# Optimization experiments

Hardware: AMD Instinct MI355X
Metric: run time of the kernel (lower is better)

Reference implementation:

```python
import jax, jax.numpy as jnp
import numpy as np

DEPTH = 6; HEADS = 6; DIM = 384; HD = DIM // HEADS
WS = 14; WINDOW_BLOCKS = (0, 1, 3, 4)
IMG = 512; PATCH = 16; GRID = IMG // PATCH        # 32x32 token grid
PRE_GRID = 14                                      # 224 // 16 pretrain grid
SCALE = HD ** -0.5


def layer_norm(x, w, b, eps=1e-5):
    u = x.mean(-1, keepdims=True)
    s = ((x - u) ** 2).mean(-1, keepdims=True)
    return (x - u) / jnp.sqrt(s + eps) * w + b


def get_rel_pos(size, rel_pos):
    # q_size == k_size here; relative coords in [0, 2*size-2]
    coords = jnp.arange(size)[:, None] - jnp.arange(size)[None, :] + (size - 1)
    return rel_pos[coords]  # (size, size, HD)


def attention(x, qkv_w, qkv_b, proj_w, proj_b, rel_h, rel_w):
    B, H, W, C = x.shape
    N = H * W
    qkv = (x.reshape(B, N, C) @ qkv_w.T + qkv_b).reshape(B, N, 3, HEADS, HD)
    qkv = jnp.moveaxis(qkv, 2, 0).transpose(0, 1, 3, 2, 4)  # (3,B,h,N,d)
    q, k, v = qkv[0], qkv[1], qkv[2]
    attn = jnp.einsum('bhqd,bhkd->bhqk', q * SCALE, k)
    # decomposed relative position bias (ViTDet add_decomposed_rel_pos)
    Rh = get_rel_pos(H, rel_h)  # (H,H,d)
    Rw = get_rel_pos(W, rel_w)  # (W,W,d)
    rq = q.reshape(B, HEADS, H, W, HD)
    bias_h = jnp.einsum('bnhwc,hkc->bnhwk', rq, Rh)  # (B,h,H,W,H)
    bias_w = jnp.einsum('bnhwc,wkc->bnhwk', rq, Rw)  # (B,h,H,W,W)
    attn = (attn.reshape(B, HEADS, H, W, H, W)
            + bias_h[..., :, None] + bias_w[..., None, :]).reshape(B, HEADS, N, N)
    attn = jax.nn.softmax(attn, axis=-1)
    out = jnp.einsum('bhqk,bhkd->bhqd', attn, v)
    out = out.transpose(0, 2, 1, 3).reshape(B, H, W, C)
    return out @ proj_w.T + proj_b


def window_partition(x, ws):
    B, H, W, C = x.shape
    pad_h = (ws - H % ws) % ws
    pad_w = (ws - W % ws) % ws
    x = jnp.pad(x, ((0, 0), (0, pad_h), (0, pad_w), (0, 0)))
    Hp, Wp = H + pad_h, W + pad_w
    x = x.reshape(B, Hp // ws, ws, Wp // ws, ws, C)
    x = x.transpose(0, 1, 3, 2, 4, 5).reshape(-1, ws, ws, C)
    return x, Hp, Wp


def window_unpartition(win, ws, Hp, Wp, H, W):
    B = win.shape[0] // ((Hp // ws) * (Wp // ws))
    x = win.reshape(B, Hp // ws, Wp // ws, ws, ws, -1)
    x = x.transpose(0, 1, 3, 2, 4, 5).reshape(B, Hp, Wp, -1)
    return x[:, :H, :W]


def block(x, p, windowed):
    shortcut = x
    x = layer_norm(x, p['n1w'], p['n1b'])
    if windowed:
        H, W = x.shape[1], x.shape[2]
        x, Hp, Wp = window_partition(x, WS)
    x = attention(x, p['qw'], p['qb'], p['pw'], p['pb'], p['rh'], p['rw'])
    if windowed:
        x = window_unpartition(x, WS, Hp, Wp, H, W)
    x = shortcut + x
    h = layer_norm(x, p['n2w'], p['n2b'])
    h = jax.nn.gelu(h @ p['f1w'].T + p['f1b'], approximate=False)
    return x + h @ p['f2w'].T + p['f2b']


def vit_forward(x, patch_w, patch_b, pos_embed, norm1_w, norm1_b, qkv_w, qkv_b,
                proj_w, proj_b, norm2_w, norm2_b, fc1_w, fc1_b, fc2_w, fc2_b,
                rel_pos_h, rel_pos_w):
    y = jax.lax.conv_general_dilated(
        x, patch_w, (PATCH, PATCH), 'VALID',
        dimension_numbers=('NCHW', 'OIHW', 'NCHW'))
    y = y.transpose(0, 2, 3, 1) + patch_b  # (B, GRID, GRID, DIM)
    # abs pos embed: bicubic resize from pretrain 14x14 grid to 32x32
    pos = pos_embed.reshape(1, PRE_GRID, PRE_GRID, DIM)
    pos = jax.image.resize(pos, (1, GRID, GRID, DIM), 'bicubic')
    y = y + pos
    for i in range(DEPTH):
        windowed = i in WINDOW_BLOCKS
        L = 2 * WS - 1 if windowed else 2 * GRID - 1
        p = dict(n1w=norm1_w[i], n1b=norm1_b[i], qw=qkv_w[i], qb=qkv_b[i],
                 pw=proj_w[i], pb=proj_b[i], rh=rel_pos_h[i, :L], rw=rel_pos_w[i, :L],
                 n2w=norm2_w[i], n2b=norm2_b[i], f1w=fc1_w[i], f1b=fc1_b[i],
                 f2w=fc2_w[i], f2b=fc2_b[i])
        y = block(y, p, windowed)
    return y.transpose(0, 3, 1, 2)  # (B, DIM, GRID, GRID) 'last_feat'


def setup_inputs() -> dict:
    key = jax.random.key(0)
    ks = jax.random.split(key, 10)
    B = 4
    std = 0.02
    f32 = jnp.float32
    return {
        'x': jax.random.normal(ks[0], (B, 3, IMG, IMG), f32),
        'patch_w': jax.random.normal(ks[1], (DIM, 3, PATCH, PATCH), f32) * 0.05,
        'patch_b': jnp.zeros((DIM,), f32),
        'pos_embed': jax.random.normal(ks[2], (1, PRE_GRID * PRE_GRID, DIM), f32) * std,
        'norm1_w': jnp.ones((DEPTH, DIM), f32),
        'norm1_b': jnp.zeros((DEPTH, DIM), f32),
        'qkv_w': jax.random.normal(ks[3], (DEPTH, 3 * DIM, DIM), f32) * std,
        'qkv_b': jnp.zeros((DEPTH, 3 * DIM), f32),
        'proj_w': jax.random.normal(ks[4], (DEPTH, DIM, DIM), f32) * std,
        'proj_b': jnp.zeros((DEPTH, DIM), f32),
        'norm2_w': jnp.ones((DEPTH, DIM), f32),
        'norm2_b': jnp.zeros((DEPTH, DIM), f32),
        'fc1_w': jax.random.normal(ks[5], (DEPTH, 4 * DIM, DIM), f32) * std,
        'fc1_b': jnp.zeros((DEPTH, 4 * DIM), f32),
        'fc2_w': jax.random.normal(ks[6], (DEPTH, DIM, 4 * DIM), f32) * std,
        'fc2_b': jnp.zeros((DEPTH, DIM), f32),
        'rel_pos_h': jax.random.normal(ks[7], (DEPTH, 2 * GRID - 1, HD), f32) * std,
        'rel_pos_w': jax.random.normal(ks[8], (DEPTH, 2 * GRID - 1, HD), f32) * std,
    }


def reference(x, patch_w, patch_b, pos_embed, norm1_w, norm1_b, qkv_w, qkv_b,
              proj_w, proj_b, norm2_w, norm2_b, fc1_w, fc1_b, fc2_w, fc2_b,
              rel_pos_h, rel_pos_w):
    return vit_forward(x, patch_w, patch_b, pos_embed, norm1_w, norm1_b, qkv_w, qkv_b,
                       proj_w, proj_b, norm2_w, norm2_b, fc1_w, fc1_b, fc2_w, fc2_b,
                       rel_pos_h, rel_pos_w)
```

## Files before the change

kernel.cpp:

```cpp
#include <hip/hip_runtime.h>
#include <math.h>

#define B_SZ 4
#define DIM 384
#define HEADS 6
#define HD 64
#define NTOK 4096
#define WS 14
#define NWIN 36
#define WTOK 196

typedef unsigned short u16;
typedef __bf16 bf16_t;
typedef bf16_t bf16x8 __attribute__((ext_vector_type(8)));
typedef float f32x4 __attribute__((ext_vector_type(4)));

__device__ __forceinline__ float bf2f(unsigned u) { return __uint_as_float(u << 16); }
__device__ __forceinline__ u16 f2bf(float f) {
    unsigned u = __float_as_uint(f);
    unsigned r = (u + 0x7fffu + ((u >> 16) & 1u)) >> 16;
    return (u16)r;
}

__device__ __forceinline__ void ldsload16(const u16* g, u16* l) {
    __builtin_amdgcn_global_load_lds(
        (const __attribute__((address_space(1))) unsigned int*)g,
        (__attribute__((address_space(3))) unsigned int*)l, 16, 0, 0);
}

__device__ __forceinline__ int swz(int r) { return (r ^ (r >> 2)) & 3; }

__device__ inline float cubic_keys(float x) {
    x = fabsf(x);
    if (x <= 1.f) return ((1.5f * x - 2.5f) * x) * x + 1.f;
    if (x < 2.f)  return ((-0.5f * x + 2.5f) * x - 4.f) * x + 2.f;
    return 0.f;
}

__global__ __launch_bounds__(256) void setup_kernel(
        const float* __restrict__ p0, const float* __restrict__ p1,
        const float* __restrict__ p2, const float* __restrict__ p3,
        const float* __restrict__ p4, const float* __restrict__ p5,
        u16* __restrict__ wb, const float* __restrict__ pe,
        float* __restrict__ posr, const float* __restrict__ x,
        u16* __restrict__ col) {
    int i = (blockIdx.x * 256 + threadIdx.x) * 4;
    if (i < 10918656) {
        const float* s; int off;
        if      (i <   294912) { s = p0; off = 0; }
        else if (i <  2949120) { s = p1; off = 294912; }
        else if (i <  3833856) { s = p2; off = 2949120; }
        else if (i <  7372800) { s = p3; off = 3833856; }
        else if (i < 10911744) { s = p4; off = 7372800; }
        else                   { s = p5; off = 10911744; }
        float4 v = *(const float4*)(s + (i - off));
        u16 o[4] = { f2bf(v.x), f2bf(v.y), f2bf(v.z), f2bf(v.w) };
        *(uint2*)(wb + i) = *(const uint2*)o;
        return;
    }
    i -= 10918656;
    if (i < 393216) {
        int c = i % 384;
        int g = i / 384;
        int gy = g / 32, gx = g % 32;
        float wy[14], wx[14];
        float sy = (gy + 0.5f) * (14.f / 32.f) - 0.5f;
        float sx = (gx + 0.5f) * (14.f / 32.f) - 0.5f;
        float toty = 0.f, totx = 0.f;
        #pragma unroll
        for (int k = 0; k < 14; ++k) {
            wy[k] = cubic_keys(sy - (float)k); toty += wy[k];
            wx[k] = cubic_keys(sx - (float)k); totx += wx[k];
        }
        float4 acc = {0.f, 0.f, 0.f, 0.f};
        #pragma unroll 1
        for (int iy = 0; iy < 14; ++iy) {
            if (wy[iy] == 0.f) continue;
            float4 row = {0.f, 0.f, 0.f, 0.f};
            for (int ix = 0; ix < 14; ++ix) {
                if (wx[ix] == 0.f) continue;
                float4 pv = *(const float4*)(pe + (iy * 14 + ix) * 384 + c);
                row.x += wx[ix] * pv.x; row.y += wx[ix] * pv.y;
                row.z += wx[ix] * pv.z; row.w += wx[ix] * pv.w;
            }
            acc.x += wy[iy] * row.x; acc.y += wy[iy] * row.y;
            acc.z += wy[iy] * row.z; acc.w += wy[iy] * row.w;
        }
        float inv = 1.f / (toty * totx);
        acc.x *= inv; acc.y *= inv; acc.z *= inv; acc.w *= inv;
        *(float4*)(posr + i) = acc;
        return;
    }
    i -= 393216;
    if (i < 3145728) {
        int kk = i % 768;
        int p  = i / 768;
        int b  = p / 1024;
        int ph = (p % 1024) / 32;
        int pw = p % 32;
        int c = kk / 256;
        int r = kk % 256;
        int ii = r / 16, j = r % 16;
        float4 v = *(const float4*)(x + (size_t)b * 3 * 512 * 512 +
                                    (size_t)c * 512 * 512 +
                                    (size_t)(ph * 16 + ii) * 512 + (pw * 16 + j));
        u16 o[4] = { f2bf(v.x), f2bf(v.y), f2bf(v.z), f2bf(v.w) };
        *(uint2*)(col + i) = *(const uint2*)o;
    }
}

__global__ __launch_bounds__(64) void epi_ln_kernel(const float* __restrict__ P,
        const float* __restrict__ bias, const float* __restrict__ posr,
        float* __restrict__ y, int addy, int nsk,
        const float* __restrict__ lw, const float* __restrict__ lb,
        u16* __restrict__ lnout, float* __restrict__ outT)
{
    int tok = blockIdx.x, t = threadIdx.x;
    size_t base = (size_t)tok * 384;
    float v[6];
    float s = 0.f;
    #pragma unroll
    for (int i = 0; i < 6; ++i) {
        int c = t + 64 * i;
        float val = bias[c];
        #pragma unroll 1
        for (int sk = 0; sk < nsk; ++sk)
            val += P[(size_t)sk * 1572864 + base + c];
        if (posr) val += posr[(size_t)(tok & 1023) * 384 + c];
        if (addy) val += y[base + c];
        v[i] = val; s += val;
    }
    if (outT) {
        int b = tok >> 10, g = tok & 1023;
        #pragma unroll
        for (int i = 0; i < 6; ++i) {
            int c = t + 64 * i;
            outT[((size_t)(b * 384 + c)) * 1024 + g] = v[i];
        }
        return;
    }
    #pragma unroll
    for (int i = 0; i < 6; ++i) y[base + t + 64 * i] = v[i];
    if (!lnout) return;
    #pragma unroll
    for (int off = 32; off > 0; off >>= 1) s += __shfl_xor(s, off);
    float mean = s * (1.f / 384.f);
    float vs = 0.f;
    #pragma unroll
    for (int i = 0; i < 6; ++i) { float d = v[i] - mean; vs += d * d; }
    #pragma unroll
    for (int off = 32; off > 0; off >>= 1) vs += __shfl_xor(vs, off);
    float inv = rsqrtf(vs * (1.f / 384.f) + 1e-5f);
    u16* orow = lnout + base;
    #pragma unroll
    for (int i = 0; i < 6; ++i) {
        int c = t + 64 * i;
        orow[c] = f2bf((v[i] - mean) * inv * lw[c] + lb[c]);
    }
}

__global__ __launch_bounds__(256) void mfma_gemm4(
        const u16* __restrict__ A, const u16* __restrict__ Wt,
        const float* __restrict__ bias,
        float* __restrict__ outf, u16* __restrict__ outb,
        float* __restrict__ outp,
        int M, int N, int K, int act, int ksplit)
{
    __shared__ u16 As[2][8192];
    __shared__ u16 Bs[2][4096];
    int t = threadIdx.x;
    int lane = t & 63, wave = t >> 6;
    int wm = (wave >> 1) * 64, wn = (wave & 1) * 32;
    int m0 = blockIdx.y * 128, n0 = blockIdx.x * 64;
    int ks = blockIdx.z * ksplit;

    int r0 = t >> 2,        c0 = ((t & 3) ^ swz(t >> 2)) * 8;
    int r1 = 64 + (t >> 2), c1 = ((t & 3) ^ swz(64 + (t >> 2))) * 8;
    const u16* a0 = A + (size_t)(m0 + r0) * K + c0;
    const u16* a1 = A + (size_t)(m0 + r1) * K + c1;
    const u16* b0 = Wt + (size_t)(n0 + r0) * K + c0;

    auto stage = [&](int k0, int buf) {
        ldsload16(a0 + k0,      &As[buf][wave * 512]);
        ldsload16(a1 + k0,      &As[buf][2048 + wave * 512]);
        ldsload16(b0 + k0,      &Bs[buf][wave * 512]);
        ldsload16(a0 + k0 + 32, &As[buf][4096 + wave * 512]);
        ldsload16(a1 + k0 + 32, &As[buf][6144 + wave * 512]);
        ldsload16(b0 + k0 + 32, &Bs[buf][2048 + wave * 512]);
    };

    f32x4 acc[4][2] = {};
    int row_a = wm + (lane & 15);
    int row_b = wn + (lane & 15);
    int lq = lane >> 4;
    int nchunks = ksplit / 64;

    stage(ks, 0);
    __syncthreads();

    for (int ci = 0; ci < nchunks; ++ci) {
        int p = ci & 1;
        bool pref = (ci + 1 < nchunks);
        if (pref) stage(ks + (ci + 1) * 64, 1 - p);
        #pragma unroll
        for (int hf = 0; hf < 2; ++hf) {
            bf16x8 af[4], bfr[2];
            #pragma unroll
            for (int i = 0; i < 4; ++i) {
                int r = row_a + i * 16;
                af[i] = *(const bf16x8*)&As[p][hf * 4096 + r * 32 + ((lq ^ swz(r)) * 8)];
            }
            #pragma unroll
            for (int j = 0; j < 2; ++j) {
                int r = row_b + j * 16;
                bfr[j] = *(const bf16x8*)&Bs[p][hf * 2048 + r * 32 + ((lq ^ swz(r)) * 8)];
            }
            #pragma unroll
            for (int i = 0; i < 4; ++i)
                #pragma unroll
                for (int j = 0; j < 2; ++j)
                    acc[i][j] = __builtin_amdgcn_mfma_f32_16x16x32_bf16(
                        af[i], bfr[j], acc[i][j], 0, 0, 0);
        }
        if (pref) __syncthreads();
    }

    int colq = lane & 15, rowq = (lane >> 4) * 4;
    if (outp) {
        float* pp = outp + (size_t)blockIdx.z * M * N;
        #pragma unroll
        for (int i = 0; i < 4; ++i) {
            #pragma unroll
            for (int rr = 0; rr < 4; ++rr) {
                int m = m0 + wm + i * 16 + rowq + rr;
                size_t mo = (size_t)m * N;
                #pragma unroll
                for (int j = 0; j < 2; ++j) {
                    int n = n0 + wn + j * 16 + colq;
                    pp[mo + n] = acc[i][j][rr];
                }
            }
        }
        return;
    }
    #pragma unroll
    for (int i = 0; i < 4; ++i) {
        #pragma unroll
        for (int rr = 0; rr < 4; ++rr) {
            int m = m0 + wm + i * 16 + rowq + rr;
            size_t mo = (size_t)m * N;
            #pragma unroll
            for (int j = 0; j < 2; ++j) {
                int n = n0 + wn + j * 16 + colq;
                float v = acc[i][j][rr] + bias[n];
                if (act)  v = 0.5f * v * (1.f + erff(v * 0.70710678118654752f));
                if (outf) outf[mo + n] = v;
                if (outb) outb[mo + n] = f2bf(v);
            }
        }
    }
}

template<int N, int W>
__global__ __launch_bounds__(256) void attn_mfma(const u16* __restrict__ qkv,
        const u16* __restrict__ qkb, const float* __restrict__ rh,
        const float* __restrict__ rw, u16* __restrict__ outb)
{
    constexpr int JS = (W == 32) ? 64 : 32;
    constexpr int L  = (W == 32) ? 63 : 27;
    constexpr int CTR = W - 1;
    __shared__ u16 KV[11776];
    __shared__ u16 bhl[64 * 66];
    __shared__ u16 bwl[64 * 66];
    __shared__ u16 Qt[64 * 66];

    u16* Pb = KV + 9216;
    u16* Rt = KV;

    int t = threadIdx.x, lane = t & 63, wave = t >> 6;
    int quad = lane >> 4, l15 = lane & 15;
    int uh = blockIdx.x, qb0 = blockIdx.y * 64;
    int h = uh % HEADS, u = uh / HEADS;
    size_t tbase = (size_t)u * 1024;
    int wb_ = u / 9, wr = u - wb_ * 9;
    int wy = wr / 3, wx = wr - wy * 3;

    auto rowptr = [&](int lq2) -> const u16* {
        if constexpr (W == 32) {
            return qkv + (tbase + lq2) * 1152;
        } else {
            int iy = lq2 / WS, ix = lq2 - iy * WS;
            int gy = wy * WS + iy, gx = wx * WS + ix;
            if (gy < 32 && gx < 32)
                return qkv + (size_t)(wb_ * 1024 + gy * 32 + gx) * 1152;
            return qkb;
        }
    };

    {
        int q = t & 63, ch0 = (t >> 6) * 16;
        int qc = qb0 + q; if (qc >= N) qc = N - 1;
        const u16* qp = rowptr(qc) + h * 64 + ch0;
        uint4 a = *(const uint4*)qp;
        uint4 b = *(const uint4*)(qp + 8);
        u16 vals[16];
        *(uint4*)vals = a; *(uint4*)(vals + 8) = b;
        #pragma unroll
        for (int c = 0; c < 16; ++c)
            Qt[(ch0 + c) * 66 + q] = ((qb0 + q) < N) ? vals[c] : (u16)0;
    }

    #pragma unroll
    for (int table = 0; table < 2; ++table) {
        __syncthreads();
        const float* tab = table ? rw : rh;
        for (int idx = t; idx < JS * 8; idx += 256) {
            int j = idx >> 3, cc0 = (idx & 7) * 8;
            u16 tmp[8];
            if (j < L) {
                const float* src = tab + (size_t)j * 64 + cc0;
                #pragma unroll
                for (int c = 0; c < 8; ++c) tmp[c] = f2bf(src[c]);
            } else {
                #pragma unroll
                for (int c = 0; c < 8; ++c) tmp[c] = 0;
            }
            *(uint4*)&Rt[j * 72 + cc0] = *(uint4*)tmp;
        }
        __syncthreads();
        if (wave < JS / 16) {
            int jt = wave;
            bf16x8 af0 = *(const bf16x8*)&Rt[(jt * 16 + l15) * 72 + quad * 8];
            bf16x8 af1 = *(const bf16x8*)&Rt[(jt * 16 + l15) * 72 + 32 + quad * 8];
            u16* dst = table ? bwl : bhl;
            #pragma unroll
            for (int qt = 0; qt < 4; ++qt) {
                bf16x8 qf0, qf1;
                u16* p0 = (u16*)&qf0; u16* p1 = (u16*)&qf1;
                #pragma unroll
                for (int z = 0; z < 8; ++z) {
                    p0[z] = Qt[(quad * 8 + z) * 66 + qt * 16 + l15];
                    p1[z] = Qt[(32 + quad * 8 + z) * 66 + qt * 16 + l15];
                }
                f32x4 acc = {};
                acc = __builtin_amdgcn_mfma_f32_16x16x32_bf16(af0, qf0, acc, 0, 0, 0);
                acc = __builtin_amdgcn_mfma_f32_16x16x32_bf16(af1, qf1, acc, 0, 0, 0);
                #pragma unroll
                for (int r = 0; r < 4; ++r)
                    dst[(qt * 16 + l15) * 66 + jt * 16 + quad * 4 + r] = f2bf(acc[r]);
            }
        }
    }
    __syncthreads();

    constexpr int NKT = (N + 31) / 32;
    {
        int pch = wave * 64 + lane;
        int key = pch >> 3;
        int c8 = (pch & 7) ^ (key & 7);
        int kc = key; if (kc >= N) kc = N - 1;
        ldsload16(rowptr(kc) + 384 + h * 64 + c8 * 8, KV + wave * 512);
        int k = t & 31, ch0v = (t >> 5) * 8;
        uint4 vv = *(const uint4*)(rowptr(k) + 768 + h * 64 + ch0v);
        u16 tmp[8]; *(uint4*)tmp = vv;
        u16* vdst = KV + 4096;
        #pragma unroll
        for (int c = 0; c < 8; ++c) vdst[(ch0v + c) * 40 + k] = tmp[c];
    }

    bf16x8 qf[2];
    #pragma unroll
    for (int hc = 0; hc < 2; ++hc) {
        u16* qv = (u16*)&qf[hc];
        #pragma unroll
        for (int j = 0; j < 8; ++j)
            qv[j] = Qt[(hc * 32 + quad * 8 + j) * 66 + wave * 16 + l15];
    }
    int qme = wave * 16 + l15;
    int qq = qb0 + qme; if (qq >= N) qq = N - 1;
    int qh = qq / W, qw = qq - qh * W;
    float bwreg[2][4];
    if constexpr (W == 32) {
        #pragma unroll
        for (int kc2 = 0; kc2 < 2; ++kc2)
            #pragma unroll
            for (int r = 0; r < 4; ++r) {
                int keyl = kc2 * 16 + quad * 4 + r;
                bwreg[kc2][r] = bf2f(bwl[qme * 66 + (qw - keyl + CTR)]);
            }
    }

    f32x4 of[4] = {};
    float lsum = 0.f;
    __syncthreads();

    for (int kt = 0; kt < NKT; ++kt) {
        int kb = kt * 32;
        int p = kt & 1;
        const u16* ksp = KV + p * 2048;
        const u16* vtp = KV + 4096 + p * 2560;
        bool pref = (kt + 1 < NKT);
        uint4 vpref;
        int kpf = t & 31, ch0v = (t >> 5) * 8;
        if (pref) {
            int kb2 = kb + 32;
            int pch = wave * 64 + lane;
            int key = pch >> 3;
            int c8 = (pch & 7) ^ (key & 7);
            int kc = kb2 + key; if (kc >= N) kc = N - 1;
            ldsload16(rowptr(kc) + 384 + h * 64 + c8 * 8,
                      KV + (1 - p) * 2048 + wave * 512);
            int kcv = kb2 + kpf; if (kcv >= N) kcv = N - 1;
            vpref = *(const uint4*)(rowptr(kcv) + 768 + h * 64 + ch0v);
        }

        f32x4 st[2] = {};
        #pragma unroll
        for (int hc = 0; hc < 2; ++hc) {
            #pragma unroll
            for (int kc2 = 0; kc2 < 2; ++kc2) {
                int key = kc2 * 16 + l15;
                int c8 = hc * 4 + quad;
                int pp = key * 8 + (c8 ^ (key & 7));
                bf16x8 kf = *(const bf16x8*)&ksp[pp * 8];
                st[kc2] = __builtin_amdgcn_mfma_f32_16x16x32_bf16(
                    kf, qf[hc], st[kc2], 0, 0, 0);
            }
        }
        float bh_t = 0.f;
        if constexpr (W == 32) bh_t = bf2f(bhl[qme * 66 + (qh - (kb >> 5) + CTR)]);
        #pragma unroll
        for (int kc2 = 0; kc2 < 2; ++kc2) {
            #pragma unroll
            for (int r = 0; r < 4; ++r) {
                int keyl = kc2 * 16 + quad * 4 + r;
                int key = kb + keyl;
                float b;
                if constexpr (W == 32) {
                    b = bh_t + bwreg[kc2][r];
                } else {
                    int kk2 = (key < N) ? key : (N - 1);
                    int kh = kk2 / W, kw = kk2 - kh * W;
                    b = bf2f(bhl[qme * 66 + (qh - kh + CTR)]) +
                        bf2f(bwl[qme * 66 + (qw - kw + CTR)]);
                }
                float pv = __expf(fmaf(st[kc2][r], 0.125f, b));
                if (key >= N) pv = 0.f;
                lsum += pv;
                Pb[wave * 640 + l15 * 40 + keyl] = f2bf(pv);
            }
        }
        bf16x8 pf = *(const bf16x8*)&Pb[wave * 640 + l15 * 40 + quad * 8];
        #pragma unroll
        for (int ca = 0; ca < 4; ++ca) {
            bf16x8 vf = *(const bf16x8*)&vtp[(ca * 16 + l15) * 40 + quad * 8];
            of[ca] = __builtin_amdgcn_mfma_f32_16x16x32_bf16(
                vf, pf, of[ca], 0, 0, 0);
        }

        if (pref) {
            u16 tmp[8]; *(uint4*)tmp = vpref;
            u16* vdst = KV + 4096 + (1 - p) * 2560;
            #pragma unroll
            for (int c = 0; c < 8; ++c) vdst[(ch0v + c) * 40 + kpf] = tmp[c];
            __syncthreads();
        }
    }

    lsum += __shfl_xor(lsum, 16);
    lsum += __shfl_xor(lsum, 32);
    float inv = 1.f / lsum;
    int q = qb0 + qme;
    if (q < N) {
        u16* op;
        if constexpr (W == 32) {
            op = outb + (tbase + q) * 384 + h * 64;
        } else {
            int iy = q / WS, ix = q - iy * WS;
            int gy = wy * WS + iy, gx = wx * WS + ix;
            if (gy >= 32 || gx >= 32) return;
            op = outb + (size_t)(wb_ * 1024 + gy * 32 + gx) * 384 + h * 64;
        }
        #pragma unroll
        for (int ca = 0; ca < 4; ++ca)
            #pragma unroll
            for (int r = 0; r < 4; ++r)
                op[ca * 16 + quad * 4 + r] = f2bf(of[ca][r] * inv);
    }
}

static inline void launch_gemm(const u16* A, const u16* W, const float* bias,
                               float* outf, u16* outb,
                               int M, int N, int K, int act, hipStream_t s) {
    dim3 g(N / 64, M / 128, 1);
    mfma_gemm4<<<g, 256, 0, s>>>(A, W, bias, outf, outb, nullptr, M, N, K, act, K);
}

static inline void launch_gemm_sk(const u16* A, const u16* W, float* P,
                                  int M, int N, int K, int SK, hipStream_t s) {
    dim3 g(N / 64, M / 128, SK);
    mfma_gemm4<<<g, 256, 0, s>>>(A, W, nullptr, nullptr, nullptr, P,
                                 M, N, K, 0, K / SK);
}

extern "C" void kernel_launch(void* const* d_in, const int* in_sizes, int n_in,
                              void* d_out, int out_size, void* d_ws, size_t ws_size,
                              hipStream_t stream) {
    const float* x      = (const float*)d_in[0];
    const float* patchw = (const float*)d_in[1];
    const float* patchb = (const float*)d_in[2];
    const float* pos    = (const float*)d_in[3];
    const float* n1w    = (const float*)d_in[4];
    const float* n1b    = (const float*)d_in[5];
    const float* qkvw   = (const float*)d_in[6];
    const float* qkvb   = (const float*)d_in[7];
    const float* pw     = (const float*)d_in[8];
    const float* pb     = (const float*)d_in[9];
    const float* n2w    = (const float*)d_in[10];
    const float* n2b    = (const float*)d_in[11];
    const float* f1w    = (const float*)d_in[12];
    const float* f1b    = (const float*)d_in[13];
    const float* f2w    = (const float*)d_in[14];
    const float* f2b    = (const float*)d_in[15];
    const float* rph    = (const float*)d_in[16];
    const float* rpw    = (const float*)d_in[17];
    float* out = (float*)d_out;

    float* y   = (float*)d_ws;
    u16* attb  = (u16*)(y + 1572864);
    u16* mlpb  = attb + 1572864;
    u16* lnb   = mlpb + 6291456;
    u16* qkvx  = lnb + 1572864;
    u16* rsrv  = qkvx + 4718592;
    u16* wb    = rsrv + 7864320;
    float* posr = (float*)(wb + 10918656);

    u16* colb  = rsrv;
    float* P_patch = (float*)attb;
    float* P_pf    = (float*)qkvx;

    u16* wb_patch = wb;
    u16* wb_qkv   = wb + 294912;
    u16* wb_pw    = wb + 2949120;
    u16* wb_f1    = wb + 3833856;
    u16* wb_f2    = wb + 7372800;
    u16* wqb      = wb + 10911744;

    setup_kernel<<<(14457600 / 4 + 255) / 256, 256, 0, stream>>>(
        patchw, qkvw, pw, f1w, f2w, qkvb, wb, pos, posr, x, colb);

    launch_gemm_sk(colb, wb_patch, P_patch, NTOK, 384, 768, 2, stream);
    epi_ln_kernel<<<NTOK, 64, 0, stream>>>(P_patch, patchb, posr, y, 0, 2,
                                           n1w, n1b, lnb, nullptr);

    for (int i = 0; i < 6; ++i) {
        bool windowed = (i == 0 || i == 1 || i == 3 || i == 4);
        const float* rh = rph + (size_t)i * 63 * 64;
        const float* rw = rpw + (size_t)i * 63 * 64;
        launch_gemm(lnb, wb_qkv + (size_t)i * 442368, qkvb + i * 1152,
                    nullptr, qkvx, NTOK, 1152, 384, 0, stream);
        if (windowed) {
            attn_mfma<WTOK, WS><<<dim3(NWIN * HEADS, 4), 256, 0, stream>>>(
                qkvx, wqb + i * 1152, rh, rw, attb);
        } else {
            attn_mfma<1024, 32><<<dim3(B_SZ * HEADS, 16), 256, 0, stream>>>(
                qkvx, wqb + i * 1152, rh, rw, attb);
        }
        launch_gemm_sk(attb, wb_pw + (size_t)i * 147456, P_pf,
                       NTOK, 384, 384, 2, stream);
        epi_ln_kernel<<<NTOK, 64, 0, stream>>>(P_pf, pb + i * 384, nullptr, y, 1, 2,
                                               n2w + i * 384, n2b + i * 384, lnb,
                                               nullptr);
        launch_gemm(lnb, wb_f1 + (size_t)i * 589824, f1b + i * 1536,
                    nullptr, mlpb, NTOK, 1536, 384, 1, stream);
        launch_gemm_sk(mlpb, wb_f2 + (size_t)i * 589824, P_pf,
                       NTOK, 384, 1536, 2, stream);
        if (i < 5)
            epi_ln_kernel<<<NTOK, 64, 0, stream>>>(P_pf, f2b + i * 384, nullptr, y,
                                                   1, 2, n1w + (i + 1) * 384,
                                                   n1b + (i + 1) * 384, lnb, nullptr);
        else
            epi_ln_kernel<<<NTOK, 64, 0, stream>>>(P_pf, f2b + i * 384, nullptr, y,
                                                   1, 2, nullptr, nullptr, nullptr,
                                                   out);
    }
}
```

Measured before the change: 762.6 us.

## Split global attention keys across two blocks and merge partial sums

Global-attention blocks now split the 1024 keys into two halves along a new grid z dimension. Each half writes unnormalized fp32 partial outputs and row sums, and a new merge kernel combines and normalizes them, doubling the block count for the low-occupancy global layers (384 to 768 blocks). The windowed path replaces per-key division for token coordinates with incrementally advanced indices and packed bf16 stores. The trade-off is an extra kernel launch and fp32 partial-buffer traffic. The merge has no max rescaling, so it relies on the existing softmax having none either.

After: 753.6 us. About the same (-1.2%).

```diff
diff --git a/kernel.cpp b/kernel.cpp
--- a/kernel.cpp
+++ b/kernel.cpp
@@ -1,4 +1,5 @@
 #include <hip/hip_runtime.h>
+#include <hip/hip_bf16.h>
 #include <math.h>
 
 #define B_SZ 4
@@ -20,6 +21,10 @@
     unsigned u = __float_as_uint(f);
     unsigned r = (u + 0x7fffu + ((u >> 16) & 1u)) >> 16;
     return (u16)r;
+}
+__device__ __forceinline__ unsigned pk2bf(float a, float b) {
+    __hip_bfloat162 h = __float22bfloat162_rn(make_float2(a, b));
+    unsigned r; __builtin_memcpy(&r, &h, 4); return r;
 }
 
 __device__ __forceinline__ void ldsload16(const u16* g, u16* l) {
@@ -264,11 +269,14 @@
 template<int N, int W>
 __global__ __launch_bounds__(256) void attn_mfma(const u16* __restrict__ qkv,
         const u16* __restrict__ qkb, const float* __restrict__ rh,
-        const float* __restrict__ rw, u16* __restrict__ outb)
+        const float* __restrict__ rw, u16* __restrict__ outb,
+        float* __restrict__ opart, float* __restrict__ lpart)
 {
     constexpr int JS = (W == 32) ? 64 : 32;
     constexpr int L  = (W == 32) ? 63 : 27;
     constexpr int CTR = W - 1;
+    constexpr int KSPAN = (W == 32) ? 512 : 224;
+    constexpr int NKT = KSPAN / 32;
     __shared__ u16 KV[11776];
     __shared__ u16 bhl[64 * 66];
     __shared__ u16 bwl[64 * 66];
@@ -280,20 +288,25 @@
     int t = threadIdx.x, lane = t & 63, wave = t >> 6;
     int quad = lane >> 4, l15 = lane & 15;
     int uh = blockIdx.x, qb0 = blockIdx.y * 64;
+    int z = (W == 32) ? blockIdx.z : 0;
+    int kstart = z * KSPAN;
     int h = uh % HEADS, u = uh / HEADS;
     size_t tbase = (size_t)u * 1024;
     int wb_ = u / 9, wr = u - wb_ * 9;
     int wy = wr / 3, wx = wr - wy * 3;
 
+    auto tok14 = [&](int iy, int ix) -> const u16* {
+        int gy = wy * WS + iy, gx = wx * WS + ix;
+        if (gy < 32 && gx < 32)
+            return qkv + (size_t)(wb_ * 1024 + gy * 32 + gx) * 1152;
+        return qkb;
+    };
     auto rowptr = [&](int lq2) -> const u16* {
         if constexpr (W == 32) {
             return qkv + (tbase + lq2) * 1152;
         } else {
             int iy = lq2 / WS, ix = lq2 - iy * WS;
-            int gy = wy * WS + iy, gx = wx * WS + ix;
-            if (gy < 32 && gx < 32)
-                return qkv + (size_t)(wb_ * 1024 + gy * 32 + gx) * 1152;
-            return qkb;
+            return tok14(iy, ix);
         }
     };
 
@@ -338,9 +351,9 @@
                 bf16x8 qf0, qf1;
                 u16* p0 = (u16*)&qf0; u16* p1 = (u16*)&qf1;
                 #pragma unroll
-                for (int z = 0; z < 8; ++z) {
-                    p0[z] = Qt[(quad * 8 + z) * 66 + qt * 16 + l15];
-                    p1[z] = Qt[(32 + quad * 8 + z) * 66 + qt * 16 + l15];
+                for (int zz = 0; zz < 8; ++zz) {
+                    p0[zz] = Qt[(quad * 8 + zz) * 66 + qt * 16 + l15];
+                    p1[zz] = Qt[(32 + quad * 8 + zz) * 66 + qt * 16 + l15];
                 }
                 f32x4 acc = {};
                 acc = __builtin_amdgcn_mfma_f32_16x16x32_bf16(af0, qf0, acc, 0, 0, 0);
@@ -353,19 +366,30 @@
     }
     __syncthreads();
 
-    constexpr int NKT = (N + 31) / 32;
+    int skey = (wave * 64 + lane) >> 3;
+    int sc8  = ((wave * 64 + lane) & 7) ^ (skey & 7);
+    int vkey = t & 31, vch0 = (t >> 5) * 8;
+    int siy = 0, six = 0, viy = 0, vix = 0;
+    if constexpr (W != 32) {
+        int k0 = kstart + skey;
+        siy = k0 / WS; six = k0 - siy * WS;
+        int k1 = kstart + vkey;
+        viy = k1 / WS; vix = k1 - viy * WS;
+    }
+    auto adv = [](int& iy, int& ix) { ix += 4; iy += 2; if (ix >= WS) { ix -= WS; ++iy; } };
+
     {
-        int pch = wave * 64 + lane;
-        int key = pch >> 3;
-        int c8 = (pch & 7) ^ (key & 7);
-        int kc = key; if (kc >= N) kc = N - 1;
-        ldsload16(rowptr(kc) + 384 + h * 64 + c8 * 8, KV + wave * 512);
-        int k = t & 31, ch0v = (t >> 5) * 8;
-        uint4 vv = *(const uint4*)(rowptr(k) + 768 + h * 64 + ch0v);
+        const u16* kp = (W == 32) ? qkv + (tbase + kstart + skey) * 1152
+                                  : tok14(siy, six);
+        ldsload16(kp + 384 + h * 64 + sc8 * 8, KV + wave * 512);
+        const u16* vp = (W == 32) ? qkv + (tbase + kstart + vkey) * 1152
+                                  : tok14(viy, vix);
+        uint4 vv = *(const uint4*)(vp + 768 + h * 64 + vch0);
         u16 tmp[8]; *(uint4*)tmp = vv;
         u16* vdst = KV + 4096;
         #pragma unroll
-        for (int c = 0; c < 8; ++c) vdst[(ch0v + c) * 40 + k] = tmp[c];
+        for (int c = 0; c < 8; ++c) vdst[(vch0 + c) * 40 + vkey] = tmp[c];
+        if constexpr (W != 32) { adv(siy, six); adv(viy, vix); }
     }
 
     bf16x8 qf[2];
@@ -380,38 +404,39 @@
     int qq = qb0 + qme; if (qq >= N) qq = N - 1;
     int qh = qq / W, qw = qq - qh * W;
     float bwreg[2][4];
-    if constexpr (W == 32) {
-        #pragma unroll
-        for (int kc2 = 0; kc2 < 2; ++kc2)
-            #pragma unroll
-            for (int r = 0; r < 4; ++r) {
-                int keyl = kc2 * 16 + quad * 4 + r;
+    int kh_[2][4], kw_[2][4];
+    #pragma unroll
+    for (int kc2 = 0; kc2 < 2; ++kc2)
+        #pragma unroll
+        for (int r = 0; r < 4; ++r) {
+            int keyl = kc2 * 16 + quad * 4 + r;
+            if constexpr (W == 32) {
                 bwreg[kc2][r] = bf2f(bwl[qme * 66 + (qw - keyl + CTR)]);
-            }
-    }
+            } else {
+                kh_[kc2][r] = keyl / WS;
+                kw_[kc2][r] = keyl - kh_[kc2][r] * WS;
+            }
+        }
 
     f32x4 of[4] = {};
     float lsum = 0.f;
     __syncthreads();
 
     for (int kt = 0; kt < NKT; ++kt) {
-        int kb = kt * 32;
+        int kb = kstart + kt * 32;
         int p = kt & 1;
         const u16* ksp = KV + p * 2048;
         const u16* vtp = KV + 4096 + p * 2560;
         bool pref = (kt + 1 < NKT);
         uint4 vpref;
-        int kpf = t & 31, ch0v = (t >> 5) * 8;
         if (pref) {
-            int kb2 = kb + 32;
-            int pch = wave * 64 + lane;
-            int key = pch >> 3;
-            int c8 = (pch & 7) ^ (key & 7);
-            int kc = kb2 + key; if (kc >= N) kc = N - 1;
-            ldsload16(rowptr(kc) + 384 + h * 64 + c8 * 8,
-                      KV + (1 - p) * 2048 + wave * 512);
-            int kcv = kb2 + kpf; if (kcv >= N) kcv = N - 1;
-            vpref = *(const uint4*)(rowptr(kcv) + 768 + h * 64 + ch0v);
+            const u16* kp = (W == 32) ? qkv + (tbase + kb + 32 + skey) * 1152
+                                      : tok14(siy, six);
+            ldsload16(kp + 384 + h * 64 + sc8 * 8, KV + (1 - p) * 2048 + wave * 512);
+            const u16* vp = (W == 32) ? qkv + (tbase + kb + 32 + vkey) * 1152
+                                      : tok14(viy, vix);
+            vpref = *(const uint4*)(vp + 768 + h * 64 + vch0);
+            if constexpr (W != 32) { adv(siy, six); adv(viy, vix); }
         }
 
         f32x4 st[2] = {};
@@ -431,24 +456,35 @@
         if constexpr (W == 32) bh_t = bf2f(bhl[qme * 66 + (qh - (kb >> 5) + CTR)]);
         #pragma unroll
         for (int kc2 = 0; kc2 < 2; ++kc2) {
+            float pv4[4];
             #pragma unroll
             for (int r = 0; r < 4; ++r) {
                 int keyl = kc2 * 16 + quad * 4 + r;
-                int key = kb + keyl;
                 float b;
                 if constexpr (W == 32) {
                     b = bh_t + bwreg[kc2][r];
                 } else {
-                    int kk2 = (key < N) ? key : (N - 1);
-                    int kh = kk2 / W, kw = kk2 - kh * W;
-                    b = bf2f(bhl[qme * 66 + (qh - kh + CTR)]) +
-                        bf2f(bwl[qme * 66 + (qw - kw + CTR)]);
+                    b = bf2f(bhl[qme * 66 + (qh - kh_[kc2][r] + CTR)]) +
+                        bf2f(bwl[qme * 66 + (qw - kw_[kc2][r] + CTR)]);
                 }
                 float pv = __expf(fmaf(st[kc2][r], 0.125f, b));
-                if (key >= N) pv = 0.f;
+                if (kb + keyl >= N) pv = 0.f;
                 lsum += pv;
-                Pb[wave * 640 + l15 * 40 + keyl] = f2bf(pv);
-            }
+                pv4[r] = pv;
+            }
+            uint2 pk;
+            pk.x = pk2bf(pv4[0], pv4[1]);
+            pk.y = pk2bf(pv4[2], pv4[3]);
+            *(uint2*)&Pb[wave * 640 + l15 * 40 + kc2 * 16 + quad * 4] = pk;
+        }
+        if constexpr (W != 32) {
+            #pragma unroll
+            for (int kc2 = 0; kc2 < 2; ++kc2)
+                #pragma unroll
+                for (int r = 0; r < 4; ++r) {
+                    kw_[kc2][r] += 4; kh_[kc2][r] += 2;
+                    if (kw_[kc2][r] >= WS) { kw_[kc2][r] -= WS; ++kh_[kc2][r]; }
+                }
         }
         bf16x8 pf = *(const bf16x8*)&Pb[wave * 640 + l15 * 40 + quad * 8];
         #pragma unroll
@@ -462,31 +498,51 @@
             u16 tmp[8]; *(uint4*)tmp = vpref;
             u16* vdst = KV + 4096 + (1 - p) * 2560;
             #pragma unroll
-            for (int c = 0; c < 8; ++c) vdst[(ch0v + c) * 40 + kpf] = tmp[c];
+            for (int c = 0; c < 8; ++c) vdst[(vch0 + c) * 40 + vkey] = tmp[c];
             __syncthreads();
         }
     }
 
     lsum += __shfl_xor(lsum, 16);
     lsum += __shfl_xor(lsum, 32);
-    float inv = 1.f / lsum;
     int q = qb0 + qme;
-    if (q < N) {
-        u16* op;
-        if constexpr (W == 32) {
-            op = outb + (tbase + q) * 384 + h * 64;
-        } else {
+    if constexpr (W == 32) {
+        size_t ridx = (size_t)z * 24576 + (size_t)uh * 1024 + q;
+        float* op = opart + ridx * 64;
+        #pragma unroll
+        for (int ca = 0; ca < 4; ++ca)
+            *(float4*)&op[ca * 16 + quad * 4] = (float4){of[ca][0], of[ca][1],
+                                                         of[ca][2], of[ca][3]};
+        if (quad == 0) lpart[ridx] = lsum;
+    } else {
+        float inv = 1.f / lsum;
+        if (q < N) {
             int iy = q / WS, ix = q - iy * WS;
             int gy = wy * WS + iy, gx = wx * WS + ix;
             if (gy >= 32 || gx >= 32) return;
-            op = outb + (size_t)(wb_ * 1024 + gy * 32 + gx) * 384 + h * 64;
-        }
-        #pragma unroll
-        for (int ca = 0; ca < 4; ++ca)
-            #pragma unroll
-            for (int r = 0; r < 4; ++r)
-                op[ca * 16 + quad * 4 + r] = f2bf(of[ca][r] * inv);
-    }
+            u16* op = outb + (size_t)(wb_ * 1024 + gy * 32 + gx) * 384 + h * 64;
+            #pragma unroll
+            for (int ca = 0; ca < 4; ++ca) {
+                uint2 pk;
+                pk.x = pk2bf(of[ca][0] * inv, of[ca][1] * inv);
+                pk.y = pk2bf(of[ca][2] * inv, of[ca][3] * inv);
+                *(uint2*)&op[ca * 16 + quad * 4] = pk;
+            }
+        }
+    }
+}
+
+__global__ __launch_bounds__(256) void attn_merge_kernel(const float* __restrict__ O,
+        const float* __restrict__ Lp, u16* __restrict__ attb)
+{
+    int t = threadIdx.x;
+    int idx = blockIdx.x * 4 + (t >> 6);
+    int ch = t & 63;
+    float o = O[(size_t)idx * 64 + ch] + O[((size_t)24576 + idx) * 64 + ch];
+    float l = Lp[idx] + Lp[24576 + idx];
+    int uh = idx >> 10, q = idx & 1023;
+    int u = uh / 6, h = uh - u * 6;
+    attb[((size_t)(u * 1024 + q)) * 384 + h * 64 + ch] = f2bf(o / l);
 }
 
 static inline void launch_gemm(const u16* A, const u16* W, const float* bias,
@@ -538,6 +594,8 @@
     u16* colb  = rsrv;
     float* P_patch = (float*)attb;
     float* P_pf    = (float*)qkvx;
+    float* Opart   = (float*)mlpb;
+    float* Lpart   = (float*)lnb;
 
     u16* wb_patch = wb;
     u16* wb_qkv   = wb + 294912;
@@ -560,11 +618,12 @@
         launch_gemm(lnb, wb_qkv + (size_t)i * 442368, qkvb + i * 1152,
                     nullptr, qkvx, NTOK, 1152, 384, 0, stream);
         if (windowed) {
-            attn_mfma<WTOK, WS><<<dim3(NWIN * HEADS, 4), 256, 0, stream>>>(
-                qkvx, wqb + i * 1152, rh, rw, attb);
+            attn_mfma<WTOK, WS><<<dim3(NWIN * HEADS, 4, 1), 256, 0, stream>>>(
+                qkvx, wqb + i * 1152, rh, rw, attb, nullptr, nullptr);
         } else {
-            attn_mfma<1024, 32><<<dim3(B_SZ * HEADS, 16), 256, 0, stream>>>(
-                qkvx, wqb + i * 1152, rh, rw, attb);
+            attn_mfma<1024, 32><<<dim3(B_SZ * HEADS, 16, 2), 256, 0, stream>>>(
+                qkvx, wqb + i * 1152, rh, rw, nullptr, Opart, Lpart);
+            attn_merge_kernel<<<6144, 256, 0, stream>>>(Opart, Lpart, attb);
         }
         launch_gemm_sk(attb, wb_pw + (size_t)i * 147456, P_pf,
                        NTOK, 384, 384, 2, stream);
```
